# Kernel optimization log

Hardware: AMD Instinct MI355X
Metric: run time of the kernel (lower is better)

Reference implementation:

```python
import jax, jax.numpy as jnp
import numpy as np

B, N, C, H = 8, 1025, 1024, 16


def setup_inputs() -> dict:
    key = jax.random.key(0)
    k1, k2, k3, k4 = jax.random.split(key, 4)
    x = jax.random.normal(k1, (B, N, C), dtype=jnp.float32)
    w_qkv = jax.random.normal(k2, (3 * C, C), dtype=jnp.float32) * (C ** -0.5)
    w_proj = jax.random.normal(k3, (C, C), dtype=jnp.float32) * (C ** -0.5)
    b_proj = jax.random.normal(k4, (C,), dtype=jnp.float32) * 0.01
    return {"x": x, "w_qkv": w_qkv, "w_proj": w_proj, "b_proj": b_proj}


def reference(x, w_qkv, w_proj, b_proj):
    b, n, c = x.shape
    hd = c // H
    scale = hd ** -0.5
    qkv = (x @ w_qkv.T).reshape(b, n, 3, H, hd).transpose(2, 0, 3, 1, 4)
    q, k, v = qkv[0], qkv[1], qkv[2]
    # standard QK attention path
    attn_ori = jax.nn.softmax(jnp.einsum('bhnd,bhmd->bhnm', q, k) * scale, axis=-1)
    # CLIP-Surgery V-V self-correlation path (settings='' -> same scale)
    attn_vv = jax.nn.softmax(jnp.einsum('bhnd,bhmd->bhnm', v, v) * scale, axis=-1)
    x_ori = jnp.einsum('bhnm,bhmd->bhnd', attn_ori, v).transpose(0, 2, 1, 3).reshape(b, n, c)
    x_new = jnp.einsum('bhnm,bhmd->bhnd', attn_vv, v).transpose(0, 2, 1, 3).reshape(b, n, c)
    out_vv = x_new @ w_proj.T + b_proj
    out_ori = x_ori @ w_proj.T + b_proj
    return (out_vv, out_ori)
```

## Files before the change

### kernel.cpp

```cpp
#include <hip/hip_runtime.h>

typedef unsigned short ushort_t;
typedef __attribute__((ext_vector_type(8))) __bf16 bf16x8;
typedef __attribute__((ext_vector_type(4))) float f32x4;

constexpr int B_ = 8, N_ = 1025, C_ = 1024, H_ = 16, HD = 64;
constexpr int M_QKV = B_ * N_;
constexpr int M_PROJ = 2 * B_ * N_;
constexpr int K_ = 1024;
constexpr int NT = 1032;
constexpr size_t S1 = (size_t)B_ * H_ * N_ * HD;
constexpr size_t VT_SZ = (size_t)B_ * H_ * HD * NT;

__device__ __forceinline__ ushort_t f2bf(float f) {
    union { float f; unsigned u; } a; a.f = f;
    unsigned r = a.u + 0x7FFFu + ((a.u >> 16) & 1u);
    return (ushort_t)(r >> 16);
}
__device__ __forceinline__ ushort_t f2bf_fast(float f) {
    return (ushort_t)((__float_as_uint(f) + 0x8000u) >> 16);
}
__device__ __forceinline__ unsigned pk2(float x, float y) {
    unsigned a = __float_as_uint(x) + 0x8000u;
    unsigned b = __float_as_uint(y) + 0x8000u;
    return (a >> 16) | (b & 0xffff0000u);
}
__device__ __forceinline__ uint4 pack8(float4 x, float4 y) {
    return make_uint4(pk2(x.x, x.y), pk2(x.z, x.w), pk2(y.x, y.y), pk2(y.z, y.w));
}

union U4 { uint4 v; ushort_t s[8]; };

__device__ __forceinline__ void gload16(const ushort_t* g, ushort_t* l) {
    __builtin_amdgcn_global_load_lds(
        (const __attribute__((address_space(1))) void*)g,
        (__attribute__((address_space(3))) void*)l, 16, 0, 0);
}

__global__ __launch_bounds__(256)
void conv_bf16(const float* __restrict__ src, ushort_t* __restrict__ dst, int n8) {
    const int i = blockIdx.x * 256 + threadIdx.x;
    if (i < n8) {
        const float4* s = (const float4*)src + 2 * (size_t)i;
        ((uint4*)dst)[i] = pack8(s[0], s[1]);
    }
}

__global__ __launch_bounds__(256)
void gemm_qkv(const ushort_t* __restrict__ A, const ushort_t* __restrict__ Bm,
              ushort_t* __restrict__ q, ushort_t* __restrict__ k,
              ushort_t* __restrict__ v, ushort_t* __restrict__ vT) {
    __shared__ ushort_t As[128 * 32];
    __shared__ ushort_t Bs[128 * 32];
    const int tid = threadIdx.x;
    const int wave = tid >> 6, lane = tid & 63;
    const int quad = lane >> 4, l16 = lane & 15;
    const int m0 = blockIdx.y * 128, n0 = blockIdx.x * 128;
    const int wm = (wave & 1) * 64, wn = (wave >> 1) * 64;

    const int col8 = (tid & 3) * 8;
    const int row0 = tid >> 2;
    const int ar0 = min(m0 + row0,      M_QKV - 1);
    const int ar1 = min(m0 + row0 + 64, M_QKV - 1);
    const ushort_t* ga0 = A + (size_t)ar0 * K_ + col8;
    const ushort_t* ga1 = A + (size_t)ar1 * K_ + col8;
    const ushort_t* gb0 = Bm + (size_t)(n0 + row0) * K_ + col8;
    const ushort_t* gb1 = Bm + (size_t)(n0 + row0 + 64) * K_ + col8;
    ushort_t* lA0 = As + tid * 8;
    ushort_t* lA1 = As + (tid + 256) * 8;
    ushort_t* lB0 = Bs + tid * 8;
    ushort_t* lB1 = Bs + (tid + 256) * 8;

    f32x4 acc[4][4] = {};

    for (int k0 = 0; k0 < K_; k0 += 32) {
        __syncthreads();
        gload16(ga0 + k0, lA0);
        gload16(ga1 + k0, lA1);
        gload16(gb0 + k0, lB0);
        gload16(gb1 + k0, lB1);
        __syncthreads();
        bf16x8 af[4], bfr[4];
#pragma unroll
        for (int i = 0; i < 4; i++) {
            af[i]  = *(const bf16x8*)(As + (wm + i * 16 + l16) * 32 + quad * 8);
            bfr[i] = *(const bf16x8*)(Bs + (wn + i * 16 + l16) * 32 + quad * 8);
        }
#pragma unroll
        for (int im = 0; im < 4; im++)
#pragma unroll
            for (int in = 0; in < 4; in++)
                acc[im][in] = __builtin_amdgcn_mfma_f32_16x16x32_bf16(af[im], bfr[in], acc[im][in], 0, 0, 0);
    }

#pragma unroll
    for (int im = 0; im < 4; im++) {
#pragma unroll
        for (int in = 0; in < 4; in++) {
            const int gcol = n0 + wn + in * 16 + l16;
            const int which = gcol >> 10;
            const int c = gcol & 1023;
            const int h = c >> 6, d = c & 63;
            ushort_t* dst = which == 0 ? q : (which == 1 ? k : v);
#pragma unroll
            for (int r = 0; r < 4; r++) {
                const int grow = m0 + wm + im * 16 + quad * 4 + r;
                if (grow < M_QKV) {
                    const int b = grow / N_;
                    const int nn = grow - b * N_;
                    const ushort_t val = f2bf(acc[im][in][r]);
                    const size_t bh = (size_t)(b * H_ + h);
                    dst[(bh * N_ + nn) * HD + d] = val;
                    if (which == 2)
                        vT[(bh * HD + d) * NT + nn] = val;
                }
            }
        }
    }
}

__global__ __launch_bounds__(256, 4)
void attn_kernel(const ushort_t* __restrict__ q, const ushort_t* __restrict__ k,
                 const ushort_t* __restrict__ v, const ushort_t* __restrict__ vT,
                 ushort_t* __restrict__ xvv, ushort_t* __restrict__ xori) {
    __shared__ ushort_t Ks[64][72];
    __shared__ ushort_t Vs[64][72];
    __shared__ ushort_t Vt[64][72];
    __shared__ ushort_t Ps[4][16][72];

    const int tid = threadIdx.x;
    const int wave = tid >> 6, lane = tid & 63;
    const int quad = lane >> 4, l16 = lane & 15;
    const int bh = blockIdx.y;
    const int b = bh >> 4, h = bh & 15;

    const size_t base  = (size_t)bh * N_ * HD;
    const size_t baseT = (size_t)bh * HD * NT;
    const int qr0 = blockIdx.x * 64 + wave * 16;

    bf16x8 qq[2], qv[2];
    {
        const int qrow = qr0 + l16;
#pragma unroll
        for (int kk = 0; kk < 2; kk++) {
            U4 uq, uv; uq.v = make_uint4(0, 0, 0, 0); uv.v = uq.v;
            if (qrow < N_) {
                uq.v = *(const uint4*)(q + base + (size_t)qrow * HD + kk * 32 + quad * 8);
                uv.v = *(const uint4*)(v + base + (size_t)qrow * HD + kk * 32 + quad * 8);
            }
            qq[kk] = *(const bf16x8*)uq.s;
            qv[kk] = *(const bf16x8*)uv.s;
        }
    }

    float l0a[4] = {0.f, 0.f, 0.f, 0.f}, l1a[4] = {0.f, 0.f, 0.f, 0.f};
    f32x4 o0[4] = {}, o1[4] = {};

    const int nkt = (N_ + 63) / 64;
    for (int kt = 0; kt < nkt; kt++) {
        const int key0 = kt * 64;
        __syncthreads();
#pragma unroll
        for (int i = 0; i < 2; i++) {
            const int c = tid + i * 256;
            const int row = c >> 3;
            const int cc = (c & 7) * 8;
            const int key = key0 + row;
            uint4 kv = make_uint4(0, 0, 0, 0), vv = kv;
            if (key < N_) {
                kv = *(const uint4*)(k + base + (size_t)key * HD + cc);
                vv = *(const uint4*)(v + base + (size_t)key * HD + cc);
            }
            uint4 tv = *(const uint4*)(vT + baseT + (size_t)row * NT + key0 + cc);
            *(uint4*)(&Ks[row][cc]) = kv;
            *(uint4*)(&Vs[row][cc]) = vv;
            *(uint4*)(&Vt[row][cc]) = tv;
        }
        __syncthreads();

#pragma unroll
        for (int path = 0; path < 2; path++) {
            f32x4 s[4];
#pragma unroll
            for (int t = 0; t < 4; t++) {
                const ushort_t (&Kt)[64][72] = (path == 0) ? Ks : Vs;
                bf16x8 b0 = *(const bf16x8*)(&Kt[t * 16 + l16][quad * 8]);
                bf16x8 b1 = *(const bf16x8*)(&Kt[t * 16 + l16][32 + quad * 8]);
                f32x4 a = {};
                a = __builtin_amdgcn_mfma_f32_16x16x32_bf16(path == 0 ? qq[0] : qv[0], b0, a, 0, 0, 0);
                a = __builtin_amdgcn_mfma_f32_16x16x32_bf16(path == 0 ? qq[1] : qv[1], b1, a, 0, 0, 0);
                const int keyg = key0 + t * 16 + l16;
                if (keyg < N_) {
#pragma unroll
                    for (int r = 0; r < 4; r++) s[t][r] = __expf(a[r] * 0.125f);
                } else {
#pragma unroll
                    for (int r = 0; r < 4; r++) s[t][r] = 0.f;
                }
            }

            float* la = (path == 0) ? l0a : l1a;
#pragma unroll
            for (int r = 0; r < 4; r++)
                la[r] += (s[0][r] + s[1][r]) + (s[2][r] + s[3][r]);

#pragma unroll
            for (int t = 0; t < 4; t++)
#pragma unroll
                for (int r = 0; r < 4; r++)
                    Ps[wave][quad * 4 + r][t * 16 + l16] = f2bf_fast(s[t][r]);

            bf16x8 pa0 = *(const bf16x8*)(&Ps[wave][l16][quad * 8]);
            bf16x8 pa1 = *(const bf16x8*)(&Ps[wave][l16][32 + quad * 8]);
#pragma unroll
            for (int t = 0; t < 4; t++) {
                bf16x8 bv0 = *(const bf16x8*)(&Vt[t * 16 + l16][quad * 8]);
                bf16x8 bv1 = *(const bf16x8*)(&Vt[t * 16 + l16][32 + quad * 8]);
                if (path == 0) {
                    o0[t] = __builtin_amdgcn_mfma_f32_16x16x32_bf16(pa0, bv0, o0[t], 0, 0, 0);
                    o0[t] = __builtin_amdgcn_mfma_f32_16x16x32_bf16(pa1, bv1, o0[t], 0, 0, 0);
                } else {
                    o1[t] = __builtin_amdgcn_mfma_f32_16x16x32_bf16(pa0, bv0, o1[t], 0, 0, 0);
                    o1[t] = __builtin_amdgcn_mfma_f32_16x16x32_bf16(pa1, bv1, o1[t], 0, 0, 0);
                }
            }
        }
    }

#pragma unroll
    for (int r = 0; r < 4; r++) {
        float L0 = l0a[r], L1 = l1a[r];
#pragma unroll
        for (int off = 1; off < 16; off <<= 1) {
            L0 += __shfl_xor(L0, off);
            L1 += __shfl_xor(L1, off);
        }
        const int row = qr0 + quad * 4 + r;
        if (row < N_) {
            const float inv0 = 1.0f / L0;
            const float inv1 = 1.0f / L1;
            const size_t rb = (size_t)(b * N_ + row) * C_ + h * HD;
#pragma unroll
            for (int t = 0; t < 4; t++) {
                const int d = t * 16 + l16;
                xori[rb + d] = f2bf(o0[t][r] * inv0);
                xvv[rb + d]  = f2bf(o1[t][r] * inv1);
            }
        }
    }
}

__global__ __launch_bounds__(256)
void gemm_proj(const ushort_t* __restrict__ A, const ushort_t* __restrict__ Bm,
               const float* __restrict__ bias, float* __restrict__ out) {
    __shared__ ushort_t As[128 * 32];
    __shared__ ushort_t Bs[128 * 32];
    const int tid = threadIdx.x;
    const int wave = tid >> 6, lane = tid & 63;
    const int quad = lane >> 4, l16 = lane & 15;
    const int m0 = blockIdx.y * 128, n0 = blockIdx.x * 128;
    const int wm = (wave & 1) * 64, wn = (wave >> 1) * 64;

    const int col8 = (tid & 3) * 8;
    const int row0 = tid >> 2;
    const int ar0 = min(m0 + row0,      M_PROJ - 1);
    const int ar1 = min(m0 + row0 + 64, M_PROJ - 1);
    const ushort_t* ga0 = A + (size_t)ar0 * K_ + col8;
    const ushort_t* ga1 = A + (size_t)ar1 * K_ + col8;
    const ushort_t* gb0 = Bm + (size_t)(n0 + row0) * K_ + col8;
    const ushort_t* gb1 = Bm + (size_t)(n0 + row0 + 64) * K_ + col8;
    ushort_t* lA0 = As + tid * 8;
    ushort_t* lA1 = As + (tid + 256) * 8;
    ushort_t* lB0 = Bs + tid * 8;
    ushort_t* lB1 = Bs + (tid + 256) * 8;

    f32x4 acc[4][4] = {};

    for (int k0 = 0; k0 < K_; k0 += 32) {
        __syncthreads();
        gload16(ga0 + k0, lA0);
        gload16(ga1 + k0, lA1);
        gload16(gb0 + k0, lB0);
        gload16(gb1 + k0, lB1);
        __syncthreads();
        bf16x8 af[4], bfr[4];
#pragma unroll
        for (int i = 0; i < 4; i++) {
            af[i]  = *(const bf16x8*)(As + (wm + i * 16 + l16) * 32 + quad * 8);
            bfr[i] = *(const bf16x8*)(Bs + (wn + i * 16 + l16) * 32 + quad * 8);
        }
#pragma unroll
        for (int im = 0; im < 4; im++)
#pragma unroll
            for (int in = 0; in < 4; in++)
                acc[im][in] = __builtin_amdgcn_mfma_f32_16x16x32_bf16(af[im], bfr[in], acc[im][in], 0, 0, 0);
    }

#pragma unroll
    for (int im = 0; im < 4; im++) {
#pragma unroll
        for (int in = 0; in < 4; in++) {
            const int gcol = n0 + wn + in * 16 + l16;
            const float bb = bias[gcol];
#pragma unroll
            for (int r = 0; r < 4; r++) {
                const int grow = m0 + wm + im * 16 + quad * 4 + r;
                if (grow < M_PROJ)
                    out[(size_t)grow * C_ + gcol] = acc[im][in][r] + bb;
            }
        }
    }
}

extern "C" void kernel_launch(void* const* d_in, const int* in_sizes, int n_in,
                              void* d_out, int out_size, void* d_ws, size_t ws_size,
                              hipStream_t stream) {
    const float* x      = (const float*)d_in[0];
    const float* w_qkv  = (const float*)d_in[1];
    const float* w_proj = (const float*)d_in[2];
    const float* b_proj = (const float*)d_in[3];
    float* out = (float*)d_out;

    ushort_t* ws = (ushort_t*)d_ws;
    ushort_t* x_bf     = ws;
    ushort_t* xvv      = ws;
    ushort_t* xori     = ws + S1;
    ushort_t* v        = ws + 2 * S1;
    ushort_t* wproj_bf = ws + 2 * S1;

    ushort_t* q        = (ushort_t*)d_out;
    ushort_t* k        = (ushort_t*)d_out + S1;
    ushort_t* vT       = (ushort_t*)d_out + 2 * S1;
    ushort_t* wqkv_bf  = (ushort_t*)d_out + 2 * S1 + VT_SZ;

    {
        const int n8x = (int)(S1 / 8);
        conv_bf16<<<(n8x + 255) / 256, 256, 0, stream>>>(x, x_bf, n8x);
        const int n8w = 3 * C_ * C_ / 8;
        conv_bf16<<<(n8w + 255) / 256, 256, 0, stream>>>(w_qkv, wqkv_bf, n8w);
    }
    {
        dim3 grid(3072 / 128, (M_QKV + 127) / 128);
        gemm_qkv<<<grid, 256, 0, stream>>>(x_bf, wqkv_bf, q, k, v, vT);
    }
    {
        dim3 grid((N_ + 63) / 64, B_ * H_);
        attn_kernel<<<grid, 256, 0, stream>>>(q, k, v, vT, xvv, xori);
    }
    {
        const int n8p = C_ * C_ / 8;
        conv_bf16<<<(n8p + 255) / 256, 256, 0, stream>>>(w_proj, wproj_bf, n8p);
    }
    {
        dim3 grid(1024 / 128, (M_PROJ + 127) / 128);
        gemm_proj<<<grid, 256, 0, stream>>>(xvv, wproj_bf, b_proj, out);
    }
}
```

Before: 414.3 us.

## Fold softmax scale into Q, reuse K smem for P, specialize tail tiles

The QKV GEMM epilogue now pre-multiplies Q by the softmax scale, which removes a multiply per score in the QK path. The attention kernel drops its separate P buffer and writes P into the K tile's shared memory after an extra barrier, to cut LDS use and allow higher occupancy. It also splits the two paths into explicit sequential blocks, adds a fast no-bounds-check load path for full key tiles, and clamps the last query block so it overlaps the previous one instead of guarding rows. The cost is an added __syncthreads per tile and some redundant recomputation of overlapping query rows in the last block.

Result: no change. 410.2 us (-1.0%).

```diff
diff --git a/kernel.cpp b/kernel.cpp
--- a/kernel.cpp
+++ b/kernel.cpp
@@ -102,13 +102,14 @@
             const int c = gcol & 1023;
             const int h = c >> 6, d = c & 63;
             ushort_t* dst = which == 0 ? q : (which == 1 ? k : v);
+            const float sc = (which == 0) ? 0.125f : 1.0f;
 #pragma unroll
             for (int r = 0; r < 4; r++) {
                 const int grow = m0 + wm + im * 16 + quad * 4 + r;
                 if (grow < M_QKV) {
                     const int b = grow / N_;
                     const int nn = grow - b * N_;
-                    const ushort_t val = f2bf(acc[im][in][r]);
+                    const ushort_t val = f2bf(acc[im][in][r] * sc);
                     const size_t bh = (size_t)(b * H_ + h);
                     dst[(bh * N_ + nn) * HD + d] = val;
                     if (which == 2)
@@ -126,7 +127,6 @@
     __shared__ ushort_t Ks[64][72];
     __shared__ ushort_t Vs[64][72];
     __shared__ ushort_t Vt[64][72];
-    __shared__ ushort_t Ps[4][16][72];
 
     const int tid = threadIdx.x;
     const int wave = tid >> 6, lane = tid & 63;
@@ -136,18 +136,19 @@
 
     const size_t base  = (size_t)bh * N_ * HD;
     const size_t baseT = (size_t)bh * HD * NT;
-    const int qr0 = blockIdx.x * 64 + wave * 16;
+    const int qstart = min((int)blockIdx.x * 64, N_ - 64);
+    const int qr0 = qstart + wave * 16;
+
+    ushort_t (*Ps)[72] = Ks;
 
     bf16x8 qq[2], qv[2];
     {
         const int qrow = qr0 + l16;
 #pragma unroll
         for (int kk = 0; kk < 2; kk++) {
-            U4 uq, uv; uq.v = make_uint4(0, 0, 0, 0); uv.v = uq.v;
-            if (qrow < N_) {
-                uq.v = *(const uint4*)(q + base + (size_t)qrow * HD + kk * 32 + quad * 8);
-                uv.v = *(const uint4*)(v + base + (size_t)qrow * HD + kk * 32 + quad * 8);
-            }
+            U4 uq, uv;
+            uq.v = *(const uint4*)(q + base + (size_t)qrow * HD + kk * 32 + quad * 8);
+            uv.v = *(const uint4*)(v + base + (size_t)qrow * HD + kk * 32 + quad * 8);
             qq[kk] = *(const bf16x8*)uq.s;
             qv[kk] = *(const bf16x8*)uv.s;
         }
@@ -155,74 +156,119 @@
 
     float l0a[4] = {0.f, 0.f, 0.f, 0.f}, l1a[4] = {0.f, 0.f, 0.f, 0.f};
     f32x4 o0[4] = {}, o1[4] = {};
+
+    const int srow = tid >> 3;
+    const int scc  = (tid & 7) * 8;
 
     const int nkt = (N_ + 63) / 64;
     for (int kt = 0; kt < nkt; kt++) {
         const int key0 = kt * 64;
-        __syncthreads();
-#pragma unroll
-        for (int i = 0; i < 2; i++) {
-            const int c = tid + i * 256;
-            const int row = c >> 3;
-            const int cc = (c & 7) * 8;
-            const int key = key0 + row;
-            uint4 kv = make_uint4(0, 0, 0, 0), vv = kv;
-            if (key < N_) {
-                kv = *(const uint4*)(k + base + (size_t)key * HD + cc);
-                vv = *(const uint4*)(v + base + (size_t)key * HD + cc);
-            }
-            uint4 tv = *(const uint4*)(vT + baseT + (size_t)row * NT + key0 + cc);
-            *(uint4*)(&Ks[row][cc]) = kv;
-            *(uint4*)(&Vs[row][cc]) = vv;
-            *(uint4*)(&Vt[row][cc]) = tv;
-        }
-        __syncthreads();
-
-#pragma unroll
-        for (int path = 0; path < 2; path++) {
-            f32x4 s[4];
-#pragma unroll
-            for (int t = 0; t < 4; t++) {
-                const ushort_t (&Kt)[64][72] = (path == 0) ? Ks : Vs;
-                bf16x8 b0 = *(const bf16x8*)(&Kt[t * 16 + l16][quad * 8]);
-                bf16x8 b1 = *(const bf16x8*)(&Kt[t * 16 + l16][32 + quad * 8]);
-                f32x4 a = {};
-                a = __builtin_amdgcn_mfma_f32_16x16x32_bf16(path == 0 ? qq[0] : qv[0], b0, a, 0, 0, 0);
-                a = __builtin_amdgcn_mfma_f32_16x16x32_bf16(path == 0 ? qq[1] : qv[1], b1, a, 0, 0, 0);
-                const int keyg = key0 + t * 16 + l16;
-                if (keyg < N_) {
-#pragma unroll
-                    for (int r = 0; r < 4; r++) s[t][r] = __expf(a[r] * 0.125f);
-                } else {
-#pragma unroll
-                    for (int r = 0; r < 4; r++) s[t][r] = 0.f;
+        const bool tail = (key0 + 64 > N_);
+        __syncthreads();
+        if (!tail) {
+#pragma unroll
+            for (int i = 0; i < 2; i++) {
+                const int row = srow + i * 32;
+                const int key = key0 + row;
+                uint4 kv = *(const uint4*)(k + base + (size_t)key * HD + scc);
+                uint4 vv = *(const uint4*)(v + base + (size_t)key * HD + scc);
+                uint4 tv = *(const uint4*)(vT + baseT + (size_t)row * NT + key0 + scc);
+                *(uint4*)(&Ks[row][scc]) = kv;
+                *(uint4*)(&Vs[row][scc]) = vv;
+                *(uint4*)(&Vt[row][scc]) = tv;
+            }
+        } else {
+#pragma unroll
+            for (int i = 0; i < 2; i++) {
+                const int row = srow + i * 32;
+                const int key = key0 + row;
+                uint4 kv = make_uint4(0, 0, 0, 0), vv = kv;
+                if (key < N_) {
+                    kv = *(const uint4*)(k + base + (size_t)key * HD + scc);
+                    vv = *(const uint4*)(v + base + (size_t)key * HD + scc);
                 }
-            }
-
-            float* la = (path == 0) ? l0a : l1a;
-#pragma unroll
-            for (int r = 0; r < 4; r++)
-                la[r] += (s[0][r] + s[1][r]) + (s[2][r] + s[3][r]);
-
+                uint4 tv = *(const uint4*)(vT + baseT + (size_t)row * NT + key0 + scc);
+                *(uint4*)(&Ks[row][scc]) = kv;
+                *(uint4*)(&Vs[row][scc]) = vv;
+                *(uint4*)(&Vt[row][scc]) = tv;
+            }
+        }
+        __syncthreads();
+
+        f32x4 s[4];
+#pragma unroll
+        for (int t = 0; t < 4; t++) {
+            bf16x8 b0 = *(const bf16x8*)(&Ks[t * 16 + l16][quad * 8]);
+            bf16x8 b1 = *(const bf16x8*)(&Ks[t * 16 + l16][32 + quad * 8]);
+            f32x4 a = {};
+            a = __builtin_amdgcn_mfma_f32_16x16x32_bf16(qq[0], b0, a, 0, 0, 0);
+            a = __builtin_amdgcn_mfma_f32_16x16x32_bf16(qq[1], b1, a, 0, 0, 0);
+            s[t] = a;
+        }
+        __syncthreads();
+
+        if (tail) {
 #pragma unroll
             for (int t = 0; t < 4; t++)
-#pragma unroll
-                for (int r = 0; r < 4; r++)
-                    Ps[wave][quad * 4 + r][t * 16 + l16] = f2bf_fast(s[t][r]);
-
-            bf16x8 pa0 = *(const bf16x8*)(&Ps[wave][l16][quad * 8]);
-            bf16x8 pa1 = *(const bf16x8*)(&Ps[wave][l16][32 + quad * 8]);
+                if (key0 + t * 16 + l16 >= N_) {
+#pragma unroll
+                    for (int r = 0; r < 4; r++) s[t][r] = -1e30f;
+                }
+        }
+#pragma unroll
+        for (int t = 0; t < 4; t++)
+#pragma unroll
+            for (int r = 0; r < 4; r++) {
+                const float p = __expf(s[t][r]);
+                l0a[r] += p;
+                Ps[wave * 16 + quad * 4 + r][t * 16 + l16] = f2bf_fast(p);
+            }
+        {
+            bf16x8 pa0 = *(const bf16x8*)(&Ps[wave * 16 + l16][quad * 8]);
+            bf16x8 pa1 = *(const bf16x8*)(&Ps[wave * 16 + l16][32 + quad * 8]);
 #pragma unroll
             for (int t = 0; t < 4; t++) {
                 bf16x8 bv0 = *(const bf16x8*)(&Vt[t * 16 + l16][quad * 8]);
                 bf16x8 bv1 = *(const bf16x8*)(&Vt[t * 16 + l16][32 + quad * 8]);
-                if (path == 0) {
-                    o0[t] = __builtin_amdgcn_mfma_f32_16x16x32_bf16(pa0, bv0, o0[t], 0, 0, 0);
-                    o0[t] = __builtin_amdgcn_mfma_f32_16x16x32_bf16(pa1, bv1, o0[t], 0, 0, 0);
-                } else {
-                    o1[t] = __builtin_amdgcn_mfma_f32_16x16x32_bf16(pa0, bv0, o1[t], 0, 0, 0);
-                    o1[t] = __builtin_amdgcn_mfma_f32_16x16x32_bf16(pa1, bv1, o1[t], 0, 0, 0);
+                o0[t] = __builtin_amdgcn_mfma_f32_16x16x32_bf16(pa0, bv0, o0[t], 0, 0, 0);
+                o0[t] = __builtin_amdgcn_mfma_f32_16x16x32_bf16(pa1, bv1, o0[t], 0, 0, 0);
+            }
+        }
+
+#pragma unroll
+        for (int t = 0; t < 4; t++) {
+            bf16x8 b0 = *(const bf16x8*)(&Vs[t * 16 + l16][quad * 8]);
+            bf16x8 b1 = *(const bf16x8*)(&Vs[t * 16 + l16][32 + quad * 8]);
+            f32x4 a = {};
+            a = __builtin_amdgcn_mfma_f32_16x16x32_bf16(qv[0], b0, a, 0, 0, 0);
+            a = __builtin_amdgcn_mfma_f32_16x16x32_bf16(qv[1], b1, a, 0, 0, 0);
+            s[t] = a;
+        }
+        if (tail) {
+#pragma unroll
+            for (int t = 0; t < 4; t++)
+                if (key0 + t * 16 + l16 >= N_) {
+#pragma unroll
+                    for (int r = 0; r < 4; r++) s[t][r] = -1e30f;
                 }
+        }
+#pragma unroll
+        for (int t = 0; t < 4; t++)
+#pragma unroll
+            for (int r = 0; r < 4; r++) {
+                const float p = __expf(s[t][r] * 0.125f);
+                l1a[r] += p;
+                Ps[wave * 16 + quad * 4 + r][t * 16 + l16] = f2bf_fast(p);
+            }
+        {
+            bf16x8 pa0 = *(const bf16x8*)(&Ps[wave * 16 + l16][quad * 8]);
+            bf16x8 pa1 = *(const bf16x8*)(&Ps[wave * 16 + l16][32 + quad * 8]);
+#pragma unroll
+            for (int t = 0; t < 4; t++) {
+                bf16x8 bv0 = *(const bf16x8*)(&Vt[t * 16 + l16][quad * 8]);
+                bf16x8 bv1 = *(const bf16x8*)(&Vt[t * 16 + l16][32 + quad * 8]);
+                o1[t] = __builtin_amdgcn_mfma_f32_16x16x32_bf16(pa0, bv0, o1[t], 0, 0, 0);
+                o1[t] = __builtin_amdgcn_mfma_f32_16x16x32_bf16(pa1, bv1, o1[t], 0, 0, 0);
             }
         }
     }
@@ -236,16 +282,14 @@
             L1 += __shfl_xor(L1, off);
         }
         const int row = qr0 + quad * 4 + r;
-        if (row < N_) {
-            const float inv0 = 1.0f / L0;
-            const float inv1 = 1.0f / L1;
-            const size_t rb = (size_t)(b * N_ + row) * C_ + h * HD;
-#pragma unroll
-            for (int t = 0; t < 4; t++) {
-                const int d = t * 16 + l16;
-                xori[rb + d] = f2bf(o0[t][r] * inv0);
-                xvv[rb + d]  = f2bf(o1[t][r] * inv1);
-            }
+        const float inv0 = 1.0f / L0;
+        const float inv1 = 1.0f / L1;
+        const size_t rb = (size_t)(b * N_ + row) * C_ + h * HD;
+#pragma unroll
+        for (int t = 0; t < 4; t++) {
+            const int d = t * 16 + l16;
+            xori[rb + d] = f2bf(o0[t][r] * inv0);
+            xvv[rb + d]  = f2bf(o1[t][r] * inv1);
         }
     }
 }
```
